# Optimization experiments

Measured on AMD Instinct MI355X. Metric: run time of the kernel, lower is better.

## Reference

```python
import jax, jax.numpy as jnp
import numpy as np

BS, N, D_FEAT, D_LINE = 32, 512, 32, 32
F_IN, F_HID, F_OUT = 64, 16, 64   # n_units
N_HEAD, N_TYPE = 8, 3
NEG_SLOPE = 0.2


def _gat_layer(h, adj_mask, v_types, w, a_src, a_dst, bias):
    # h: (b, n, f_in); w: (T, H, f_in, f_out); v_types: (b, n) int
    # project with every type's weight (cheap: T*H*f_out small), then gather per node
    h_all = jnp.einsum('bnf,thfo->bthno', h, w)                 # (b, T, H, n, f_out)
    idx = v_types[:, None, None, :, None].astype(jnp.int32)     # (b,1,1,n,1)
    h_prime = jnp.take_along_axis(h_all, idx, axis=1)[:, 0]     # (b, H, n, f_out)
    t = jnp.tanh(h_prime)
    a_s = jnp.einsum('bhno,ho->bhn', t, a_src[..., 0])          # (b, H, n)
    a_d = jnp.einsum('bhno,ho->bhn', t, a_dst[..., 0])
    attn = a_s[:, :, :, None] + a_d[:, :, None, :]              # (b, H, n, n)
    attn = jnp.where(attn >= 0, attn, NEG_SLOPE * attn)         # leaky_relu
    attn = jnp.where(adj_mask[:, None, :, :], attn, -jnp.inf)
    attn = jax.nn.softmax(attn, axis=-1)
    out = jnp.einsum('bhnm,bhmo->bhno', attn, h_prime) + bias   # (b, H, n, f_out)
    return out, attn


def setup_inputs() -> dict:
    key = jax.random.key(0)
    ks = jax.random.split(key, 16)
    features = jax.random.normal(ks[0], (BS, N, D_FEAT), jnp.float32)
    line_emb = jax.random.normal(ks[1], (BS, N, D_LINE), jnp.float32)
    adj = jax.random.randint(ks[2], (BS, N, N), 0, 2, jnp.int32)
    adj = adj.at[:, jnp.arange(N), jnp.arange(N)].set(1)  # self loops -> no empty rows
    v_types = jax.random.randint(ks[3], (BS, N), 0, N_TYPE, jnp.int32)
    svm_features = jax.random.normal(ks[4], (BS, 10), jnp.float32)

    def xavier(k, shape):
        fan_in, fan_out = shape[-2], shape[-1]
        lim = np.sqrt(6.0 / (fan_in + fan_out))
        return jax.random.uniform(k, shape, jnp.float32, -lim, lim)

    params = dict(
        w1=xavier(ks[5], (N_TYPE, N_HEAD, F_IN, F_HID)),
        a_src1=xavier(ks[6], (N_HEAD, F_HID, 1)),
        a_dst1=xavier(ks[7], (N_HEAD, F_HID, 1)),
        b1=jnp.zeros((F_HID,), jnp.float32),
        w2=xavier(ks[8], (N_TYPE, 1, N_HEAD * F_HID, F_OUT)),
        a_src2=xavier(ks[9], (1, F_OUT, 1)),
        a_dst2=xavier(ks[10], (1, F_OUT, 1)),
        b2=jnp.zeros((F_OUT,), jnp.float32),
        fc1_w=xavier(ks[11], (F_OUT, 3 * F_OUT)), fc1_b=jnp.zeros((3 * F_OUT,), jnp.float32),
        fc2_w=xavier(ks[12], (3 * F_OUT, F_OUT)), fc2_b=jnp.zeros((F_OUT,), jnp.float32),
        fc3_w=xavier(ks[13], (F_OUT, 2)), fc3_b=jnp.zeros((2,), jnp.float32),
    )
    return dict(features=features, adj=adj, bs=BS, num_v=N, svm_features=svm_features,
                line_emb=line_emb, v_types=v_types, **params)


def reference(features, adj, bs, num_v, svm_features, line_emb, v_types,
              w1, a_src1, a_dst1, b1, w2, a_src2, a_dst2, b2,
              fc1_w, fc1_b, fc2_w, fc2_b, fc3_w, fc3_b):
    adj_mask = adj > 0
    emb = jnp.concatenate([features, line_emb], axis=2)         # (b, n, F_IN)
    b, n = adj.shape[:2]
    x, attn1 = _gat_layer(emb, adj_mask, v_types, w1, a_src1, a_dst1, b1)
    x = jax.nn.elu(jnp.transpose(x, (0, 2, 1, 3)).reshape(b, n, -1))  # (b, n, H*F_HID)
    # dropout inactive at eval
    x, _ = _gat_layer(x, adj_mask, v_types, w2, a_src2, a_dst2, b2)   # (b, 1, n, F_OUT)
    x = jax.nn.elu(x)[:, 0]                                           # squeeze -> (b, n, F_OUT)
    left, right = x[:, 0, :], x[:, 1, :]
    v_sim_mul = left * right
    v = jax.nn.relu(v_sim_mul @ fc1_w + fc1_b)
    v = jax.nn.relu(v @ fc2_w + fc2_b)
    scores = v @ fc3_w + fc3_b
    return jax.nn.log_softmax(scores, axis=1), v_sim_mul, attn1
```

## Files before the change

kernel.cpp:

```cpp
#include <hip/hip_runtime.h>
#include <math.h>

#define BS 32
#define NV 512
#define NHEAD 8
#define FHID 16
#define FOUT 64
#define NTYPE 3
#define NEG_SLOPE 0.2f

#define OUT_VSIM   64
#define OUT_ATTN   2112

typedef __attribute__((ext_vector_type(8))) short bh8;
typedef __attribute__((ext_vector_type(4))) float f32x4;

__device__ __forceinline__ float wave_red_max(float v) {
#pragma unroll
    for (int m = 1; m < 64; m <<= 1) v = fmaxf(v, __shfl_xor(v, m));
    return v;
}
__device__ __forceinline__ float wave_red_sum(float v) {
#pragma unroll
    for (int m = 1; m < 64; m <<= 1) v += __shfl_xor(v, m);
    return v;
}
__device__ __forceinline__ ushort f2bf(float x) {
    union { float f; unsigned u; } v; v.f = x;
    return (ushort)((v.u + 0x7FFFu + ((v.u >> 16) & 1u)) >> 16);
}

__global__ __launch_bounds__(256) void transpose_w2(const float* __restrict__ w2,
                                                    float* __restrict__ w2T) {
    int idx = blockIdx.x * 256 + threadIdx.x;
    if (idx < 3 * 64 * 128) {
        int t = idx >> 13, rem = idx & 8191, o = rem >> 7, f = rem & 127;
        w2T[idx] = w2[((size_t)t * 128 + f) * 64 + o];
    }
}

__global__ __launch_bounds__(256) void gat1_transform_v3(
    const float* __restrict__ features, const float* __restrict__ line_emb,
    const int* __restrict__ v_types, const float* __restrict__ w1,
    const float* __restrict__ a_src1, const float* __restrict__ a_dst1,
    float* __restrict__ hpT_g, float* __restrict__ as1, float* __restrict__ ad1)
{
    int chunk = blockIdx.x & 7;
    int bh = blockIdx.x >> 3;
    int b = bh >> 3, h = bh & 7;
    int nb = chunk * 64;
    __shared__ float wT[3 * 16 * 68];
    __shared__ float emb[64 * 68];
    __shared__ float tpo[16 * 68];
    __shared__ int vt[64];
    int tid = threadIdx.x;

    for (int e = tid; e < 3 * 16 * 64; e += 256) {
        int t = e >> 10, rem = e & 1023, o = rem >> 6, k = rem & 63;
        wT[(t * 16 + o) * 68 + k] = w1[(((size_t)t * 8 + h) * 64 + k) * 16 + o];
    }
    int node0 = b * NV + nb;
    for (int e = tid; e < 64 * 64; e += 256) {
        int n = e >> 6, k = e & 63;
        float v = (k < 32) ? features[(size_t)(node0 + n) * 32 + k]
                           : line_emb[(size_t)(node0 + n) * 32 + (k - 32)];
        emb[n * 68 + k] = v;
    }
    if (tid < 64) vt[tid] = v_types[node0 + tid];
    __syncthreads();

    int o = tid & 15, nl = tid >> 4;
    float asw = a_src1[h * 16 + o], adw = a_dst1[h * 16 + o];
#pragma unroll
    for (int sub = 0; sub < 4; ++sub) {
        int n = sub * 16 + nl;
        int tt = vt[n];
        const float4* ep = (const float4*)&emb[n * 68];
        const float4* wp = (const float4*)&wT[(tt * 16 + o) * 68];
        float acc = 0.f;
#pragma unroll
        for (int kc = 0; kc < 16; ++kc) {
            float4 ev = ep[kc], wv = wp[kc];
            acc += ev.x * wv.x + ev.y * wv.y + ev.z * wv.z + ev.w * wv.w;
        }
        tpo[o * 68 + n] = acc;
        float th = tanhf(acc);
        float ps = th * asw, pd = th * adw;
#pragma unroll
        for (int m = 1; m < 16; m <<= 1) { ps += __shfl_xor(ps, m); pd += __shfl_xor(pd, m); }
        if (o == 0) {
            as1[(size_t)bh * NV + nb + n] = ps;
            ad1[(size_t)bh * NV + nb + n] = pd;
        }
    }
    __syncthreads();
    int o2 = tid >> 4, c = tid & 15;
    float4 v = *(const float4*)&tpo[o2 * 68 + c * 4];
    *(float4*)&hpT_g[((size_t)bh * 16 + o2) * NV + nb + c * 4] = v;
}

#define RPB 16
#define HS 520

__global__ __launch_bounds__(256) void gat1_attn_v3(
    const float* __restrict__ hpT_g, const float* __restrict__ as1,
    const float* __restrict__ ad1, const int* __restrict__ adj,
    const float* __restrict__ b1,
    float* __restrict__ attn_out, float* __restrict__ x1)
{
    __shared__ ushort hpb[16 * HS];
    __shared__ ushort pb[RPB * HS];
    __shared__ float partial[4][16][16];

    int bh = blockIdx.x >> 5;
    int i0 = (blockIdx.x & 31) * RPB;
    int b = bh >> 3, h = bh & 7;
    int tid = threadIdx.x;

    const float* src = hpT_g + (size_t)bh * 16 * NV;
#pragma unroll
    for (int k = 0; k < 8; ++k) {
        int flat = k * 1024 + tid * 4;
        float4 v = *(const float4*)(src + flat);
        int o = flat >> 9, n = flat & 511;
        ushort4 u; u.x = f2bf(v.x); u.y = f2bf(v.y); u.z = f2bf(v.z); u.w = f2bf(v.w);
        *(ushort4*)&hpb[o * HS + n] = u;
    }

    int wave = tid >> 6, lane = tid & 63;

    const float4* adp4 = (const float4*)(ad1 + (size_t)bh * NV);
    float4 d0 = adp4[lane * 2], d1 = adp4[lane * 2 + 1];
    const int* adjb = adj + (size_t)b * NV * NV;

#pragma unroll
    for (int rr = 0; rr < 4; ++rr) {
        int rl = wave * 4 + rr;
        int i = i0 + rl;
        float a_si = as1[(size_t)bh * NV + i];
        const int4* mrow = (const int4*)(adjb + (size_t)i * NV);
        int4 m0 = mrow[lane * 2], m1 = mrow[lane * 2 + 1];
        float s[8];
        s[0] = a_si + d0.x; s[1] = a_si + d0.y; s[2] = a_si + d0.z; s[3] = a_si + d0.w;
        s[4] = a_si + d1.x; s[5] = a_si + d1.y; s[6] = a_si + d1.z; s[7] = a_si + d1.w;
        int mk[8] = {m0.x, m0.y, m0.z, m0.w, m1.x, m1.y, m1.z, m1.w};
        float mx = -INFINITY;
#pragma unroll
        for (int k = 0; k < 8; ++k) {
            float v = s[k];
            v = (v >= 0.f) ? v : NEG_SLOPE * v;
            v = (mk[k] > 0) ? v : -INFINITY;
            s[k] = v;
            mx = fmaxf(mx, v);
        }
        mx = wave_red_max(mx);
        float sum = 0.f;
#pragma unroll
        for (int k = 0; k < 8; ++k) { s[k] = __expf(s[k] - mx); sum += s[k]; }
        sum = wave_red_sum(sum);
        float inv = 1.f / sum;
#pragma unroll
        for (int k = 0; k < 8; ++k) s[k] *= inv;

        float4* arow = (float4*)(attn_out + ((size_t)bh * NV + i) * NV);
        float4 pa = {s[0], s[1], s[2], s[3]};
        float4 pv = {s[4], s[5], s[6], s[7]};
        arow[lane * 2] = pa;
        arow[lane * 2 + 1] = pv;
        ushort4 u0 = {f2bf(s[0]), f2bf(s[1]), f2bf(s[2]), f2bf(s[3])};
        ushort4 u1 = {f2bf(s[4]), f2bf(s[5]), f2bf(s[6]), f2bf(s[7])};
        *(ushort4*)&pb[rl * HS + lane * 8] = u0;
        *(ushort4*)&pb[rl * HS + lane * 8 + 4] = u1;
    }
    __syncthreads();

    int row16 = lane & 15, kg = lane >> 4;
    f32x4 acc = {0.f, 0.f, 0.f, 0.f};
#pragma unroll
    for (int c = 0; c < 4; ++c) {
        int k0 = (wave * 4 + c) * 32 + kg * 8;
        bh8 a = *(const bh8*)&pb[row16 * HS + k0];
        bh8 bf = *(const bh8*)&hpb[row16 * HS + k0];
        acc = __builtin_amdgcn_mfma_f32_16x16x32_bf16(a, bf, acc, 0, 0, 0);
    }
    *(float4*)&partial[wave][row16][kg * 4] = *(float4*)&acc;
    __syncthreads();

    {
        int r = tid >> 4, o = tid & 15;
        float v = partial[0][o][r] + partial[1][o][r]
                + partial[2][o][r] + partial[3][o][r] + b1[o];
        v = (v > 0.f) ? v : (__expf(v) - 1.f);
        x1[((size_t)b * NV + i0 + r) * (NHEAD * FHID) + h * FHID + o] = v;
    }
}

__global__ __launch_bounds__(256) void gat2_transform_v2(
    const float* __restrict__ x1, const int* __restrict__ v_types,
    const float* __restrict__ w2T, const float* __restrict__ a_src2,
    const float* __restrict__ a_dst2,
    float* __restrict__ hp2, float* __restrict__ as2, float* __restrict__ ad2)
{
    int blk = blockIdx.x;
    int b = blk >> 4, chunk = blk & 15;
    int node0 = b * NV + chunk * 32;
    __shared__ float xin[32 * 132];
    __shared__ int vt[32];
    int tid = threadIdx.x;
    for (int e = tid; e < 32 * 128; e += 256) {
        int n = e >> 7, f = e & 127;
        xin[n * 132 + f] = x1[(size_t)(node0 + n) * 128 + f];
    }
    if (tid < 32) vt[tid] = v_types[node0 + tid];
    __syncthreads();

    int o = tid & 63, nl = tid >> 6;
    float asw = a_src2[o], adw = a_dst2[o];
#pragma unroll 2
    for (int pass = 0; pass < 8; ++pass) {
        int n = pass * 4 + nl;
        int tt = vt[n];
        const float4* xp = (const float4*)&xin[n * 132];
        const float4* wp = (const float4*)(w2T + ((size_t)tt * 64 + o) * 128);
        float acc = 0.f;
#pragma unroll
        for (int fc = 0; fc < 32; ++fc) {
            float4 xv = xp[fc], wv = wp[fc];
            acc += xv.x * wv.x + xv.y * wv.y + xv.z * wv.z + xv.w * wv.w;
        }
        hp2[(size_t)(node0 + n) * 64 + o] = acc;
        float th = tanhf(acc);
        float ps = wave_red_sum(th * asw);
        float pd = wave_red_sum(th * adw);
        if (o == 0) { as2[node0 + n] = ps; ad2[node0 + n] = pd; }
    }
}

__global__ __launch_bounds__(512) void head_v2(
    const float* __restrict__ hp2, const float* __restrict__ as2,
    const float* __restrict__ ad2, const int* __restrict__ adj,
    const float* __restrict__ b2,
    const float* __restrict__ fc1_w, const float* __restrict__ fc1_b,
    const float* __restrict__ fc2_w, const float* __restrict__ fc2_b,
    const float* __restrict__ fc3_w, const float* __restrict__ fc3_b,
    float* __restrict__ d_out)
{
    int b = blockIdx.x;
    __shared__ float p2[2][NV];
    __shared__ float partial[2 * 4 * 64];
    __shared__ float lr[2][64];
    __shared__ float vsim[64];
    __shared__ float v1[192];
    __shared__ float v2s[64];
    int tid = threadIdx.x, wave = tid >> 6, lane = tid & 63;

    if ((wave & 3) == 0) {
        int i = wave >> 2;
        float a_si = as2[(size_t)b * NV + i];
        const float4* adp4 = (const float4*)(ad2 + (size_t)b * NV);
        float4 d0 = adp4[lane * 2], d1 = adp4[lane * 2 + 1];
        const int4* mrow = (const int4*)(adj + ((size_t)b * NV + i) * NV);
        int4 m0 = mrow[lane * 2], m1 = mrow[lane * 2 + 1];
        float s[8];
        s[0] = a_si + d0.x; s[1] = a_si + d0.y; s[2] = a_si + d0.z; s[3] = a_si + d0.w;
        s[4] = a_si + d1.x; s[5] = a_si + d1.y; s[6] = a_si + d1.z; s[7] = a_si + d1.w;
        int mk[8] = {m0.x, m0.y, m0.z, m0.w, m1.x, m1.y, m1.z, m1.w};
        float mx = -INFINITY;
#pragma unroll
        for (int k = 0; k < 8; ++k) {
            float v = s[k];
            v = (v >= 0.f) ? v : NEG_SLOPE * v;
            v = (mk[k] > 0) ? v : -INFINITY;
            s[k] = v; mx = fmaxf(mx, v);
        }
        mx = wave_red_max(mx);
        float sum = 0.f;
#pragma unroll
        for (int k = 0; k < 8; ++k) { s[k] = __expf(s[k] - mx); sum += s[k]; }
        sum = wave_red_sum(sum);
        float inv = 1.f / sum;
#pragma unroll
        for (int k = 0; k < 8; ++k) p2[i][lane * 8 + k] = s[k] * inv;
    }
    __syncthreads();

    {
        int i = tid >> 8, g = (tid >> 6) & 3, o = tid & 63;
        float acc = 0.f;
        const float* hb = hp2 + ((size_t)b * NV + g * 128) * 64 + o;
#pragma unroll 8
        for (int jj = 0; jj < 128; ++jj)
            acc += p2[i][g * 128 + jj] * hb[(size_t)jj * 64];
        partial[(i * 4 + g) * 64 + o] = acc;
    }
    __syncthreads();
    if (tid < 128) {
        int i = tid >> 6, o = tid & 63;
        float v = partial[i * 256 + o] + partial[i * 256 + 64 + o]
                + partial[i * 256 + 128 + o] + partial[i * 256 + 192 + o] + b2[o];
        v = (v > 0.f) ? v : (__expf(v) - 1.f);
        lr[i][o] = v;
    }
    __syncthreads();
    if (tid < 64) {
        float v = lr[0][tid] * lr[1][tid];
        vsim[tid] = v;
        d_out[OUT_VSIM + (size_t)b * 64 + tid] = v;
    }
    __syncthreads();
    if (tid < 192) {
        float a = fc1_b[tid];
        for (int k = 0; k < 64; ++k) a += vsim[k] * fc1_w[k * 192 + tid];
        v1[tid] = fmaxf(a, 0.f);
    }
    __syncthreads();
    if (tid < 64) {
        float a = fc2_b[tid];
        for (int k = 0; k < 192; ++k) a += v1[k] * fc2_w[k * 64 + tid];
        v2s[tid] = fmaxf(a, 0.f);
    }
    __syncthreads();
    if (tid == 0) {
        float s0 = fc3_b[0], s1 = fc3_b[1];
        for (int k = 0; k < 64; ++k) { s0 += v2s[k] * fc3_w[k * 2]; s1 += v2s[k] * fc3_w[k * 2 + 1]; }
        float mm = fmaxf(s0, s1);
        float l = logf(__expf(s0 - mm) + __expf(s1 - mm));
        d_out[(size_t)b * 2 + 0] = s0 - mm - l;
        d_out[(size_t)b * 2 + 1] = s1 - mm - l;
    }
}

extern "C" void kernel_launch(void* const* d_in, const int* in_sizes, int n_in,
                              void* d_out, int out_size, void* d_ws, size_t ws_size,
                              hipStream_t stream) {
    const float* features = (const float*)d_in[0];
    const int*   adj      = (const int*)d_in[1];
    const float* line_emb = (const float*)d_in[5];
    const int*   v_types  = (const int*)d_in[6];
    const float* w1       = (const float*)d_in[7];
    const float* a_src1   = (const float*)d_in[8];
    const float* a_dst1   = (const float*)d_in[9];
    const float* b1       = (const float*)d_in[10];
    const float* w2       = (const float*)d_in[11];
    const float* a_src2   = (const float*)d_in[12];
    const float* a_dst2   = (const float*)d_in[13];
    const float* b2       = (const float*)d_in[14];
    const float* fc1_w    = (const float*)d_in[15];
    const float* fc1_b    = (const float*)d_in[16];
    const float* fc2_w    = (const float*)d_in[17];
    const float* fc2_b    = (const float*)d_in[18];
    const float* fc3_w    = (const float*)d_in[19];
    const float* fc3_b    = (const float*)d_in[20];

    float* out = (float*)d_out;
    float* ws = (float*)d_ws;
    float* hpT = ws;
    float* as1 = hpT + (size_t)BS * NHEAD * 16 * NV;
    float* ad1 = as1 + (size_t)BS * NHEAD * NV;
    float* x1  = ad1 + (size_t)BS * NHEAD * NV;
    float* hp2 = x1 + (size_t)BS * NV * NHEAD * FHID;
    float* as2 = hp2 + (size_t)BS * NV * FOUT;
    float* ad2 = as2 + (size_t)BS * NV;
    float* w2T = ad2 + (size_t)BS * NV;

    hipLaunchKernelGGL(transpose_w2, dim3(96), dim3(256), 0, stream, w2, w2T);

    hipLaunchKernelGGL(gat1_transform_v3, dim3(BS * NHEAD * (NV / 64)), dim3(256), 0, stream,
                       features, line_emb, v_types, w1, a_src1, a_dst1, hpT, as1, ad1);

    hipLaunchKernelGGL(gat1_attn_v3, dim3(BS * NHEAD * (NV / RPB)), dim3(256), 0, stream,
                       hpT, as1, ad1, adj, b1, out + OUT_ATTN, x1);

    hipLaunchKernelGGL(gat2_transform_v2, dim3(BS * (NV / 32)), dim3(256), 0, stream,
                       x1, v_types, w2T, a_src2, a_dst2, hp2, as2, ad2);

    hipLaunchKernelGGL(head_v2, dim3(BS), dim3(512), 0, stream,
                       hp2, as2, ad2, adj, b2,
                       fc1_w, fc1_b, fc2_w, fc2_b, fc3_w, fc3_b, out);
}
```

Measured before the change: 492.5 us.

## Pack adjacency into bitmasks and register-block the layer-2 transform

```diff
diff --git a/kernel.cpp b/kernel.cpp
--- a/kernel.cpp
+++ b/kernel.cpp
@@ -36,6 +36,26 @@
     if (idx < 3 * 64 * 128) {
         int t = idx >> 13, rem = idx & 8191, o = rem >> 7, f = rem & 127;
         w2T[idx] = w2[((size_t)t * 128 + f) * 64 + o];
+    }
+}
+
+__global__ __launch_bounds__(256) void build_maskbits(
+    const int* __restrict__ adj, unsigned long long* __restrict__ maskb)
+{
+    int row = blockIdx.x * 4 + (threadIdx.x >> 6);
+    int lane = threadIdx.x & 63;
+    const int4* a4 = (const int4*)(adj + (size_t)row * NV);
+#pragma unroll
+    for (int q = 0; q < 2; ++q) {
+        int4 v = a4[q * 64 + lane];
+        unsigned long long b0 = __ballot(v.x > 0);
+        unsigned long long b1 = __ballot(v.y > 0);
+        unsigned long long b2 = __ballot(v.z > 0);
+        unsigned long long b3 = __ballot(v.w > 0);
+        if (lane == 0) {
+            unsigned long long* dst = maskb + (size_t)row * 8 + q * 4;
+            dst[0] = b0; dst[1] = b1; dst[2] = b2; dst[3] = b3;
+        }
     }
 }
 
@@ -102,9 +122,9 @@
 #define RPB 16
 #define HS 520
 
-__global__ __launch_bounds__(256) void gat1_attn_v3(
+__global__ __launch_bounds__(256) void gat1_attn_v4(
     const float* __restrict__ hpT_g, const float* __restrict__ as1,
-    const float* __restrict__ ad1, const int* __restrict__ adj,
+    const float* __restrict__ ad1, const unsigned long long* __restrict__ maskb,
     const float* __restrict__ b1,
     float* __restrict__ attn_out, float* __restrict__ x1)
 {
@@ -130,47 +150,46 @@
     int wave = tid >> 6, lane = tid & 63;
 
     const float4* adp4 = (const float4*)(ad1 + (size_t)bh * NV);
-    float4 d0 = adp4[lane * 2], d1 = adp4[lane * 2 + 1];
-    const int* adjb = adj + (size_t)b * NV * NV;
+    float4 d0 = adp4[lane];
+    float4 d1 = adp4[64 + lane];
+    const unsigned long long* mbb = maskb + (size_t)b * NV * 8;
 
 #pragma unroll
     for (int rr = 0; rr < 4; ++rr) {
         int rl = wave * 4 + rr;
         int i = i0 + rl;
         float a_si = as1[(size_t)bh * NV + i];
-        const int4* mrow = (const int4*)(adjb + (size_t)i * NV);
-        int4 m0 = mrow[lane * 2], m1 = mrow[lane * 2 + 1];
+        const unsigned long long* mrow = mbb + (size_t)i * 8;
         float s[8];
         s[0] = a_si + d0.x; s[1] = a_si + d0.y; s[2] = a_si + d0.z; s[3] = a_si + d0.w;
         s[4] = a_si + d1.x; s[5] = a_si + d1.y; s[6] = a_si + d1.z; s[7] = a_si + d1.w;
-        int mk[8] = {m0.x, m0.y, m0.z, m0.w, m1.x, m1.y, m1.z, m1.w};
         float mx = -INFINITY;
 #pragma unroll
-        for (int k = 0; k < 8; ++k) {
-            float v = s[k];
+        for (int k2 = 0; k2 < 8; ++k2) {
+            float v = s[k2];
             v = (v >= 0.f) ? v : NEG_SLOPE * v;
-            v = (mk[k] > 0) ? v : -INFINITY;
-            s[k] = v;
+            v = ((mrow[k2] >> lane) & 1ull) ? v : -INFINITY;
+            s[k2] = v;
             mx = fmaxf(mx, v);
         }
         mx = wave_red_max(mx);
         float sum = 0.f;
 #pragma unroll
-        for (int k = 0; k < 8; ++k) { s[k] = __expf(s[k] - mx); sum += s[k]; }
+        for (int k2 = 0; k2 < 8; ++k2) { s[k2] = __expf(s[k2] - mx); sum += s[k2]; }
         sum = wave_red_sum(sum);
         float inv = 1.f / sum;
 #pragma unroll
-        for (int k = 0; k < 8; ++k) s[k] *= inv;
+        for (int k2 = 0; k2 < 8; ++k2) s[k2] *= inv;
 
         float4* arow = (float4*)(attn_out + ((size_t)bh * NV + i) * NV);
         float4 pa = {s[0], s[1], s[2], s[3]};
         float4 pv = {s[4], s[5], s[6], s[7]};
-        arow[lane * 2] = pa;
-        arow[lane * 2 + 1] = pv;
+        arow[lane] = pa;
+        arow[64 + lane] = pv;
         ushort4 u0 = {f2bf(s[0]), f2bf(s[1]), f2bf(s[2]), f2bf(s[3])};
         ushort4 u1 = {f2bf(s[4]), f2bf(s[5]), f2bf(s[6]), f2bf(s[7])};
-        *(ushort4*)&pb[rl * HS + lane * 8] = u0;
-        *(ushort4*)&pb[rl * HS + lane * 8 + 4] = u1;
+        *(ushort4*)&pb[rl * HS + lane * 4] = u0;
+        *(ushort4*)&pb[rl * HS + 256 + lane * 4] = u1;
     }
     __syncthreads();
 
@@ -195,44 +214,58 @@
     }
 }
 
-__global__ __launch_bounds__(256) void gat2_transform_v2(
+#define CNB 64
+__global__ __launch_bounds__(256) void gat2_transform_v3(
     const float* __restrict__ x1, const int* __restrict__ v_types,
     const float* __restrict__ w2T, const float* __restrict__ a_src2,
     const float* __restrict__ a_dst2,
     float* __restrict__ hp2, float* __restrict__ as2, float* __restrict__ ad2)
 {
-    int blk = blockIdx.x;
-    int b = blk >> 4, chunk = blk & 15;
-    int node0 = b * NV + chunk * 32;
-    __shared__ float xin[32 * 132];
-    __shared__ int vt[32];
+    int node0 = blockIdx.x * CNB;
+    __shared__ float xin[CNB * 132];
+    __shared__ int vt[CNB];
     int tid = threadIdx.x;
-    for (int e = tid; e < 32 * 128; e += 256) {
-        int n = e >> 7, f = e & 127;
-        xin[n * 132 + f] = x1[(size_t)(node0 + n) * 128 + f];
-    }
-    if (tid < 32) vt[tid] = v_types[node0 + tid];
+    for (int e = tid; e < CNB * 32; e += 256) {
+        int n = e >> 5, fc4 = e & 31;
+        *(float4*)&xin[n * 132 + fc4 * 4] =
+            *(const float4*)&x1[(size_t)(node0 + n) * 128 + fc4 * 4];
+    }
+    if (tid < CNB) vt[tid] = v_types[node0 + tid];
     __syncthreads();
 
     int o = tid & 63, nl = tid >> 6;
+    int ttn[16];
+#pragma unroll
+    for (int nn = 0; nn < 16; ++nn) ttn[nn] = vt[nl * 16 + nn];
+
+    float acc[16];
+#pragma unroll
+    for (int nn = 0; nn < 16; ++nn) acc[nn] = 0.f;
+
+    const float4* w4 = (const float4*)w2T;
+    for (int fc4 = 0; fc4 < 32; ++fc4) {
+        float4 w0 = w4[(0 * 64 + o) * 32 + fc4];
+        float4 wA = w4[(1 * 64 + o) * 32 + fc4];
+        float4 wB = w4[(2 * 64 + o) * 32 + fc4];
+#pragma unroll
+        for (int nn = 0; nn < 16; ++nn) {
+            int n = nl * 16 + nn;
+            float4 xv = *(const float4*)&xin[n * 132 + fc4 * 4];
+            int tt = ttn[nn];
+            float4 wv = (tt == 0) ? w0 : (tt == 1) ? wA : wB;
+            acc[nn] += xv.x * wv.x + xv.y * wv.y + xv.z * wv.z + xv.w * wv.w;
+        }
+    }
+
     float asw = a_src2[o], adw = a_dst2[o];
-#pragma unroll 2
-    for (int pass = 0; pass < 8; ++pass) {
-        int n = pass * 4 + nl;
-        int tt = vt[n];
-        const float4* xp = (const float4*)&xin[n * 132];
-        const float4* wp = (const float4*)(w2T + ((size_t)tt * 64 + o) * 128);
-        float acc = 0.f;
-#pragma unroll
-        for (int fc = 0; fc < 32; ++fc) {
-            float4 xv = xp[fc], wv = wp[fc];
-            acc += xv.x * wv.x + xv.y * wv.y + xv.z * wv.z + xv.w * wv.w;
-        }
-        hp2[(size_t)(node0 + n) * 64 + o] = acc;
-        float th = tanhf(acc);
+#pragma unroll
+    for (int nn = 0; nn < 16; ++nn) {
+        int n = node0 + nl * 16 + nn;
+        hp2[(size_t)n * 64 + o] = acc[nn];
+        float th = tanhf(acc[nn]);
         float ps = wave_red_sum(th * asw);
         float pd = wave_red_sum(th * adw);
-        if (o == 0) { as2[node0 + n] = ps; ad2[node0 + n] = pd; }
+        if (o == 0) { as2[n] = ps; ad2[n] = pd; }
     }
 }
 
@@ -362,16 +395,20 @@
     float* as2 = hp2 + (size_t)BS * NV * FOUT;
     float* ad2 = as2 + (size_t)BS * NV;
     float* w2T = ad2 + (size_t)BS * NV;
+    unsigned long long* maskb = (unsigned long long*)(w2T + 3 * 64 * 128);
 
     hipLaunchKernelGGL(transpose_w2, dim3(96), dim3(256), 0, stream, w2, w2T);
+
+    hipLaunchKernelGGL(build_maskbits, dim3(BS * NV / 4), dim3(256), 0, stream,
+                       adj, maskb);
 
     hipLaunchKernelGGL(gat1_transform_v3, dim3(BS * NHEAD * (NV / 64)), dim3(256), 0, stream,
                        features, line_emb, v_types, w1, a_src1, a_dst1, hpT, as1, ad1);
 
-    hipLaunchKernelGGL(gat1_attn_v3, dim3(BS * NHEAD * (NV / RPB)), dim3(256), 0, stream,
-                       hpT, as1, ad1, adj, b1, out + OUT_ATTN, x1);
-
-    hipLaunchKernelGGL(gat2_transform_v2, dim3(BS * (NV / 32)), dim3(256), 0, stream,
+    hipLaunchKernelGGL(gat1_attn_v4, dim3(BS * NHEAD * (NV / RPB)), dim3(256), 0, stream,
+                       hpT, as1, ad1, maskb, b1, out + OUT_ATTN, x1);
+
+    hipLaunchKernelGGL(gat2_transform_v3, dim3(BS * NV / CNB), dim3(256), 0, stream,
                        x1, v_types, w2T, a_src2, a_dst2, hp2, as2, ad2);
 
     hipLaunchKernelGGL(head_v2, dim3(BS), dim3(512), 0, stream,
```

After: 422.9 us. 14.1% less time.
